# Optimization experiments

Hardware: AMD Instinct MI355X
Metric: run time of the kernel (lower is better)

## Reference

```python
import jax, jax.numpy as jnp
import numpy as np

H = 128  # hidden size
I = 4    # input size
B = 256  # batch
T = 512  # seq len


def setup_inputs() -> dict:
    key = jax.random.key(0)
    ks = jax.random.split(key, 9)
    k = 1.0 / np.sqrt(H)  # PyTorch LSTM init: U(-1/sqrt(H), 1/sqrt(H))
    u = lambda kk, shape: jax.random.uniform(kk, shape, jnp.float32, -k, k)
    return {
        "x": jax.random.normal(ks[0], (B, T, I), jnp.float32),
        "Wih_f": u(ks[1], (4 * H, I)),
        "Whh_f": u(ks[2], (4 * H, H)),
        "bih_f": u(ks[3], (4 * H,)),
        "bhh_f": u(ks[4], (4 * H,)),
        "Wih_b": u(ks[5], (4 * H, I)),
        "Whh_b": u(ks[6], (4 * H, H)),
        "bih_b": u(ks[7], (4 * H,)),
        "bhh_b": u(ks[8], (4 * H,)),
    }


def _lstm_final_h(xt, Wih, Whh, bih, bhh):
    # xt: [T, B, I]. Returns final hidden state h_T: [B, H].
    # Precompute input projection for all timesteps (batched GEMM).
    xw = jnp.einsum("tbi,gi->tbg", xt, Wih) + (bih + bhh)  # [T, B, 4H]
    h0 = jnp.zeros((xt.shape[1], H), xt.dtype)
    c0 = jnp.zeros((xt.shape[1], H), xt.dtype)

    def step(carry, xw_t):
        h, c = carry
        gates = xw_t + h @ Whh.T  # [B, 4H]
        i, f, g, o = jnp.split(gates, 4, axis=-1)  # PyTorch gate order i,f,g,o
        i = jax.nn.sigmoid(i)
        f = jax.nn.sigmoid(f)
        g = jnp.tanh(g)
        o = jax.nn.sigmoid(o)
        c = f * c + i * g
        h = o * jnp.tanh(c)
        return (h, c), None

    (h_T, _), _ = jax.lax.scan(step, (h0, c0), xw)
    return h_T


def reference(x, Wih_f, Whh_f, bih_f, bhh_f, Wih_b, Whh_b, bih_b, bhh_b):
    xt = jnp.swapaxes(x, 0, 1)  # [T, B, I]
    h_fwd = _lstm_final_h(xt, Wih_f, Whh_f, bih_f, bhh_f)          # forward direction
    h_bwd = _lstm_final_h(xt[::-1], Wih_b, Whh_b, bih_b, bhh_b)    # backward direction
    # h_n: [2, B, H] -> transpose(0,1) -> [B, 2, H] -> reshape [B, 2H]
    return jnp.concatenate([h_fwd, h_bwd], axis=-1)
```

## Files before the change

### kernel.cpp

```cpp
#include <hip/hip_runtime.h>
#include <hip/hip_bf16.h>

typedef _Float16 f16;
typedef _Float16 f16x8 __attribute__((ext_vector_type(8)));
typedef float    f32x4 __attribute__((ext_vector_type(4)));

#define HDIM 128
#define IDIM 4
#define TLEN 512

__device__ __forceinline__ float sigm(float x){
  return 1.0f / (1.0f + __expf(-x));
}
__device__ __forceinline__ float tanh_fast(float x){
  float t = fabsf(x);
  float e = __expf(-2.0f * t);
  float r = (1.0f - e) / (1.0f + e);
  return copysignf(r, x);
}

__global__ __launch_bounds__(512, 2) void bilstm_mfma2(
    const float* __restrict__ x,
    const float* __restrict__ Wih_f, const float* __restrict__ Whh_f,
    const float* __restrict__ bih_f, const float* __restrict__ bhh_f,
    const float* __restrict__ Wih_b, const float* __restrict__ Whh_b,
    const float* __restrict__ bih_b, const float* __restrict__ bhh_b,
    float* __restrict__ out)
{
  __shared__ float xs[2][TLEN*IDIM];
  __shared__ float xw[2][4*HDIM][2];
  __shared__ __align__(16) f16 ha[2][4][64][8];

  const int tid = threadIdx.x;
  const int w   = tid >> 6;
  const int l   = tid & 63;
  const int c16 = l & 15;
  const int dir = blockIdx.x >> 7;
  const int b0  = (blockIdx.x & 127) * 2;

  const float* Wih = dir ? Wih_b : Wih_f;
  const float* Whh = dir ? Whh_b : Whh_f;
  const float* bih = dir ? bih_b : bih_f;
  const float* bhh = dir ? bhh_b : bhh_f;

  f16x8 bfrag[4][4];
  #pragma unroll
  for (int t = 0; t < 4; ++t){
    const int gn = t*128 + w*16 + c16;
    #pragma unroll
    for (int ks = 0; ks < 4; ++ks){
      const float* p = Whh + gn*HDIM + ks*32 + (l>>4)*8;
      float4 qa = ((const float4*)p)[0];
      float4 qb = ((const float4*)p)[1];
      f16x8 v = { (f16)qa.x,(f16)qa.y,(f16)qa.z,(f16)qa.w,
                  (f16)qb.x,(f16)qb.y,(f16)qb.z,(f16)qb.w };
      bfrag[t][ks] = v;
    }
  }
  #pragma unroll
  for (int t = 0; t < 4; ++t)
    #pragma unroll
    for (int ks = 0; ks < 4; ++ks)
      asm("" : "+v"(bfrag[t][ks]));

  const float4 wiv = *(const float4*)(Wih + tid*IDIM);
  const float bias = bih[tid] + bhh[tid];

  {
    const float4* src0 = (const float4*)(x + (size_t)(b0+0)*TLEN*IDIM);
    const float4* src1 = (const float4*)(x + (size_t)(b0+1)*TLEN*IDIM);
    ((float4*)xs[0])[tid] = src0[tid];
    ((float4*)xs[1])[tid] = src1[tid];
  }
  {
    int* hz = (int*)ha;
    hz[tid] = 0; hz[tid+512] = 0; hz[tid+1024] = 0; hz[tid+1536] = 0;
  }
  {
    const int tt0 = dir ? (TLEN-1) : 0;
    float4 xv0 = *(const float4*)(x + ((size_t)(b0+0)*TLEN + tt0)*IDIM);
    float4 xv1 = *(const float4*)(x + ((size_t)(b0+1)*TLEN + tt0)*IDIM);
    xw[0][tid][0] = bias + wiv.x*xv0.x + wiv.y*xv0.y + wiv.z*xv0.z + wiv.w*xv0.w;
    xw[0][tid][1] = bias + wiv.x*xv1.x + wiv.y*xv1.y + wiv.z*xv1.z + wiv.w*xv1.w;
  }
  __syncthreads();

  float c = 0.0f, hout = 0.0f;
  const int chainbit = (l >> 4) & 1;

  for (int s = 0; s < TLEN; ++s){
    const int rb = s & 1, wb = rb ^ 1;

    f16x8 a0 = *(const f16x8*)&ha[rb][0][l][0];
    f16x8 a1 = *(const f16x8*)&ha[rb][1][l][0];
    f16x8 a2 = *(const f16x8*)&ha[rb][2][l][0];
    f16x8 a3 = *(const f16x8*)&ha[rb][3][l][0];

    f32x4 acc[4];
    #pragma unroll
    for (int t = 0; t < 4; ++t){
      float2 p = *(const float2*)&xw[rb][t*128 + w*16 + c16][0];
      f32x4 z = { p.x, p.y, 0.f, 0.f };
      acc[t] = z;
      asm("" : "+v"(acc[t]));
    }

    {
      const int ttn = (dir ? (TLEN-2-s) : (s+1)) & (TLEN-1);
      const float4 xv0 = ((const float4*)xs[0])[ttn];
      const float4 xv1 = ((const float4*)xs[1])[ttn];
      float q0 = bias + wiv.x*xv0.x + wiv.y*xv0.y + wiv.z*xv0.z + wiv.w*xv0.w;
      float q1 = bias + wiv.x*xv1.x + wiv.y*xv1.y + wiv.z*xv1.z + wiv.w*xv1.w;
      xw[wb][tid][0] = q0;
      xw[wb][tid][1] = q1;
    }

    #pragma unroll
    for (int t = 0; t < 4; ++t){
      acc[t] = __builtin_amdgcn_mfma_f32_16x16x32_f16(a0, bfrag[t][0], acc[t], 0, 0, 0);
      acc[t] = __builtin_amdgcn_mfma_f32_16x16x32_f16(a1, bfrag[t][1], acc[t], 0, 0, 0);
      acc[t] = __builtin_amdgcn_mfma_f32_16x16x32_f16(a2, bfrag[t][2], acc[t], 0, 0, 0);
      acc[t] = __builtin_amdgcn_mfma_f32_16x16x32_f16(a3, bfrag[t][3], acc[t], 0, 0, 0);
      asm("" : "+v"(acc[t]));
    }

    float val[4];
    #pragma unroll
    for (int t = 0; t < 4; ++t){
      int pv = __builtin_amdgcn_ds_bpermute(c16 << 2, __float_as_int(acc[t].y));
      val[t] = chainbit ? __int_as_float(pv) : acc[t].x;
    }
    float iv = sigm(val[0]);
    float fv = sigm(val[1]);
    float gv = tanh_fast(val[2]);
    float ov = sigm(val[3]);
    c    = fv*c + iv*gv;
    hout = ov * tanh_fast(c);

    if (l < 32){
      const int G = (l >> 4) + ((2*w + (c16 >> 3)) & 3) * 16;
      ha[wb][w>>1][G][c16 & 7] = (f16)hout;
    }
    __syncthreads();
  }

  if (l < 32){
    out[(size_t)(b0 + (l>>4))*(2*HDIM) + dir*HDIM + w*16 + c16] = hout;
  }
}

extern "C" void kernel_launch(void* const* d_in, const int* in_sizes, int n_in,
                              void* d_out, int out_size, void* d_ws, size_t ws_size,
                              hipStream_t stream)
{
  const float* x     = (const float*)d_in[0];
  const float* Wih_f = (const float*)d_in[1];
  const float* Whh_f = (const float*)d_in[2];
  const float* bih_f = (const float*)d_in[3];
  const float* bhh_f = (const float*)d_in[4];
  const float* Wih_b = (const float*)d_in[5];
  const float* Whh_b = (const float*)d_in[6];
  const float* bih_b = (const float*)d_in[7];
  const float* bhh_b = (const float*)d_in[8];

  bilstm_mfma2<<<dim3(256), dim3(512), 0, stream>>>(
      x, Wih_f, Whh_f, bih_f, bhh_f, Wih_b, Whh_b, bih_b, bhh_b,
      (float*)d_out);
}
```

Measured before the change: 473.9 us.

## Fold input projection and bias into an extra MFMA K-slice per step

The per-step input projection (x·Wih + bias), previously computed with scalar FMAs into a shared double buffer, now comes from a fifth MFMA. The A fragment carries x in fp16 plus a constant 1 for the bias, and the B fragment carries Wih and the combined bias. This removes the xw shared-memory write/read traffic and scalar work from the recurrent critical path, at the cost of one extra MFMA per gate tile and fp16 precision for x and the bias. The loop is also unrolled by two to make the buffer indices constants, and tanh is rewritten in a shorter form without abs/copysign.

```diff
diff --git a/kernel.cpp b/kernel.cpp
--- a/kernel.cpp
+++ b/kernel.cpp
@@ -3,6 +3,7 @@
 
 typedef _Float16 f16;
 typedef _Float16 f16x8 __attribute__((ext_vector_type(8)));
+typedef _Float16 f16x4 __attribute__((ext_vector_type(4)));
 typedef float    f32x4 __attribute__((ext_vector_type(4)));
 
 #define HDIM 128
@@ -13,13 +14,10 @@
   return 1.0f / (1.0f + __expf(-x));
 }
 __device__ __forceinline__ float tanh_fast(float x){
-  float t = fabsf(x);
-  float e = __expf(-2.0f * t);
-  float r = (1.0f - e) / (1.0f + e);
-  return copysignf(r, x);
+  return 1.0f - 2.0f / (1.0f + __expf(2.0f*x));
 }
 
-__global__ __launch_bounds__(512, 2) void bilstm_mfma2(
+__global__ __launch_bounds__(512, 2) void bilstm_mfma3(
     const float* __restrict__ x,
     const float* __restrict__ Wih_f, const float* __restrict__ Whh_f,
     const float* __restrict__ bih_f, const float* __restrict__ bhh_f,
@@ -27,8 +25,7 @@
     const float* __restrict__ bih_b, const float* __restrict__ bhh_b,
     float* __restrict__ out)
 {
-  __shared__ float xs[2][TLEN*IDIM];
-  __shared__ float xw[2][4*HDIM][2];
+  __shared__ __align__(16) f16 xs16[2][TLEN][IDIM];
   __shared__ __align__(16) f16 ha[2][4][64][8];
 
   const int tid = threadIdx.x;
@@ -43,7 +40,7 @@
   const float* bih = dir ? bih_b : bih_f;
   const float* bhh = dir ? bhh_b : bhh_f;
 
-  f16x8 bfrag[4][4];
+  f16x8 bfrag[4][5];
   #pragma unroll
   for (int t = 0; t < 4; ++t){
     const int gn = t*128 + w*16 + c16;
@@ -56,93 +53,91 @@
                   (f16)qb.x,(f16)qb.y,(f16)qb.z,(f16)qb.w };
       bfrag[t][ks] = v;
     }
+    f16x8 v4 = (f16x8)(f16)0.0f;
+    if (l < 16){
+      const float4 wq = *(const float4*)(Wih + gn*IDIM);
+      const float bb = bih[gn] + bhh[gn];
+      v4[0] = (f16)wq.x; v4[1] = (f16)wq.y;
+      v4[2] = (f16)wq.z; v4[3] = (f16)wq.w;
+      v4[4] = (f16)bb;
+    }
+    bfrag[t][4] = v4;
   }
   #pragma unroll
   for (int t = 0; t < 4; ++t)
     #pragma unroll
-    for (int ks = 0; ks < 4; ++ks)
+    for (int ks = 0; ks < 5; ++ks)
       asm("" : "+v"(bfrag[t][ks]));
-
-  const float4 wiv = *(const float4*)(Wih + tid*IDIM);
-  const float bias = bih[tid] + bhh[tid];
 
   {
     const float4* src0 = (const float4*)(x + (size_t)(b0+0)*TLEN*IDIM);
     const float4* src1 = (const float4*)(x + (size_t)(b0+1)*TLEN*IDIM);
-    ((float4*)xs[0])[tid] = src0[tid];
-    ((float4*)xs[1])[tid] = src1[tid];
+    float4 v0 = src0[tid], v1 = src1[tid];
+    f16x4 h0 = { (f16)v0.x, (f16)v0.y, (f16)v0.z, (f16)v0.w };
+    f16x4 h1 = { (f16)v1.x, (f16)v1.y, (f16)v1.z, (f16)v1.w };
+    *(f16x4*)&xs16[0][tid][0] = h0;
+    *(f16x4*)&xs16[1][tid][0] = h1;
   }
   {
     int* hz = (int*)ha;
     hz[tid] = 0; hz[tid+512] = 0; hz[tid+1024] = 0; hz[tid+1536] = 0;
   }
-  {
-    const int tt0 = dir ? (TLEN-1) : 0;
-    float4 xv0 = *(const float4*)(x + ((size_t)(b0+0)*TLEN + tt0)*IDIM);
-    float4 xv1 = *(const float4*)(x + ((size_t)(b0+1)*TLEN + tt0)*IDIM);
-    xw[0][tid][0] = bias + wiv.x*xv0.x + wiv.y*xv0.y + wiv.z*xv0.z + wiv.w*xv0.w;
-    xw[0][tid][1] = bias + wiv.x*xv1.x + wiv.y*xv1.y + wiv.z*xv1.z + wiv.w*xv1.w;
-  }
   __syncthreads();
 
   float c = 0.0f, hout = 0.0f;
   const int chainbit = (l >> 4) & 1;
+  int tt = dir ? (TLEN-1) : 0;
+  const int dt = dir ? -1 : 1;
 
-  for (int s = 0; s < TLEN; ++s){
-    const int rb = s & 1, wb = rb ^ 1;
+  const int Gw  = (l >> 4) + ((2*w + (c16 >> 3)) & 3) * 16;
+  const int kse = w >> 1;
+  const int ew  = c16 & 7;
 
-    f16x8 a0 = *(const f16x8*)&ha[rb][0][l][0];
-    f16x8 a1 = *(const f16x8*)&ha[rb][1][l][0];
-    f16x8 a2 = *(const f16x8*)&ha[rb][2][l][0];
-    f16x8 a3 = *(const f16x8*)&ha[rb][3][l][0];
+#define STEP(RB, WB)                                                          \
+  {                                                                           \
+    f16x8 a0 = *(const f16x8*)&ha[RB][0][l][0];                               \
+    f16x8 a1 = *(const f16x8*)&ha[RB][1][l][0];                               \
+    f16x8 a2 = *(const f16x8*)&ha[RB][2][l][0];                               \
+    f16x8 a3 = *(const f16x8*)&ha[RB][3][l][0];                               \
+    f16x4 xq0 = *(const f16x4*)&xs16[0][tt][0];                               \
+    f16x4 xq1 = *(const f16x4*)&xs16[1][tt][0];                               \
+    f16x4 zq  = (f16x4)(f16)0.0f;                                             \
+    f16x4 sel = (l == 0) ? xq0 : ((l == 1) ? xq1 : zq);                       \
+    f16x8 a4  = (f16x8)(f16)0.0f;                                             \
+    a4[0] = sel[0]; a4[1] = sel[1]; a4[2] = sel[2]; a4[3] = sel[3];           \
+    a4[4] = (l < 2) ? (f16)1.0f : (f16)0.0f;                                  \
+    f32x4 zero4 = { 0.f, 0.f, 0.f, 0.f };                                     \
+    f32x4 acc[4];                                                             \
+    _Pragma("unroll")                                                         \
+    for (int t = 0; t < 4; ++t){                                              \
+      acc[t] = __builtin_amdgcn_mfma_f32_16x16x32_f16(a0, bfrag[t][0], zero4, 0,0,0); \
+      acc[t] = __builtin_amdgcn_mfma_f32_16x16x32_f16(a1, bfrag[t][1], acc[t], 0,0,0); \
+      acc[t] = __builtin_amdgcn_mfma_f32_16x16x32_f16(a2, bfrag[t][2], acc[t], 0,0,0); \
+      acc[t] = __builtin_amdgcn_mfma_f32_16x16x32_f16(a3, bfrag[t][3], acc[t], 0,0,0); \
+      acc[t] = __builtin_amdgcn_mfma_f32_16x16x32_f16(a4, bfrag[t][4], acc[t], 0,0,0); \
+    }                                                                         \
+    float val[4];                                                             \
+    _Pragma("unroll")                                                         \
+    for (int t = 0; t < 4; ++t){                                              \
+      int pv = __builtin_amdgcn_ds_bpermute(c16 << 2, __float_as_int(acc[t].y)); \
+      val[t] = chainbit ? __int_as_float(pv) : acc[t].x;                      \
+    }                                                                         \
+    float iv = sigm(val[0]);                                                  \
+    float fv = sigm(val[1]);                                                  \
+    float gv = tanh_fast(val[2]);                                             \
+    float ov = sigm(val[3]);                                                  \
+    c    = fv*c + iv*gv;                                                      \
+    hout = ov * tanh_fast(c);                                                 \
+    if (l < 32) ha[WB][kse][Gw][ew] = (f16)hout;                              \
+    tt += dt;                                                                 \
+    __syncthreads();                                                          \
+  }
 
-    f32x4 acc[4];
-    #pragma unroll
-    for (int t = 0; t < 4; ++t){
-      float2 p = *(const float2*)&xw[rb][t*128 + w*16 + c16][0];
-      f32x4 z = { p.x, p.y, 0.f, 0.f };
-      acc[t] = z;
-      asm("" : "+v"(acc[t]));
-    }
-
-    {
-      const int ttn = (dir ? (TLEN-2-s) : (s+1)) & (TLEN-1);
-      const float4 xv0 = ((const float4*)xs[0])[ttn];
-      const float4 xv1 = ((const float4*)xs[1])[ttn];
-      float q0 = bias + wiv.x*xv0.x + wiv.y*xv0.y + wiv.z*xv0.z + wiv.w*xv0.w;
-      float q1 = bias + wiv.x*xv1.x + wiv.y*xv1.y + wiv.z*xv1.z + wiv.w*xv1.w;
-      xw[wb][tid][0] = q0;
-      xw[wb][tid][1] = q1;
-    }
-
-    #pragma unroll
-    for (int t = 0; t < 4; ++t){
-      acc[t] = __builtin_amdgcn_mfma_f32_16x16x32_f16(a0, bfrag[t][0], acc[t], 0, 0, 0);
-      acc[t] = __builtin_amdgcn_mfma_f32_16x16x32_f16(a1, bfrag[t][1], acc[t], 0, 0, 0);
-      acc[t] = __builtin_amdgcn_mfma_f32_16x16x32_f16(a2, bfrag[t][2], acc[t], 0, 0, 0);
-      acc[t] = __builtin_amdgcn_mfma_f32_16x16x32_f16(a3, bfrag[t][3], acc[t], 0, 0, 0);
-      asm("" : "+v"(acc[t]));
-    }
-
-    float val[4];
-    #pragma unroll
-    for (int t = 0; t < 4; ++t){
-      int pv = __builtin_amdgcn_ds_bpermute(c16 << 2, __float_as_int(acc[t].y));
-      val[t] = chainbit ? __int_as_float(pv) : acc[t].x;
-    }
-    float iv = sigm(val[0]);
-    float fv = sigm(val[1]);
-    float gv = tanh_fast(val[2]);
-    float ov = sigm(val[3]);
-    c    = fv*c + iv*gv;
-    hout = ov * tanh_fast(c);
-
-    if (l < 32){
-      const int G = (l >> 4) + ((2*w + (c16 >> 3)) & 3) * 16;
-      ha[wb][w>>1][G][c16 & 7] = (f16)hout;
-    }
-    __syncthreads();
+  for (int s = 0; s < TLEN; s += 2){
+    STEP(0, 1)
+    STEP(1, 0)
   }
+#undef STEP
 
   if (l < 32){
     out[(size_t)(b0 + (l>>4))*(2*HDIM) + dir*HDIM + w*16 + c16] = hout;
@@ -163,7 +158,7 @@
   const float* bih_b = (const float*)d_in[7];
   const float* bhh_b = (const float*)d_in[8];
 
-  bilstm_mfma2<<<dim3(256), dim3(512), 0, stream>>>(
+  bilstm_mfma3<<<dim3(256), dim3(512), 0, stream>>>(
       x, Wih_f, Whh_f, bih_f, bhh_f, Wih_b, Whh_b, bih_b, bhh_b,
       (float*)d_out);
 }
```

Result: faster. 437.1 us (-7.8%).
